# Optimization experiments

Measured on AMD Instinct MI355X. Metric: run time of the kernel, lower is better.

Reference implementation:

```python
import jax, jax.numpy as jnp
import numpy as np

N, E, D_IN, D_HID, D_OUT = 50000, 800000, 128, 128, 64

def setup_inputs() -> dict:
    key = jax.random.key(0)
    ks = jax.random.split(key, 20)
    inp = {
        'x': jax.random.normal(ks[0], (N, D_IN), dtype=jnp.float32),
        'edge_index': jax.random.randint(ks[1], (2, E), 0, N, dtype=jnp.int64),
        'edge_attr': jax.random.normal(ks[2], (E, 16), dtype=jnp.float32),
        'edge_weight': jax.random.uniform(ks[3], (E,), dtype=jnp.float32),
    }
    dims = [(D_IN, D_HID), (D_HID, D_HID), (D_HID, D_OUT)]
    for i, (di, do) in enumerate(dims):
        s = 1.0 / np.sqrt(di)
        inp[f'Wl{i}'] = jax.random.uniform(ks[4 + 5 * i], (di, do), minval=-s, maxval=s, dtype=jnp.float32)
        inp[f'bl{i}'] = jnp.zeros((do,), dtype=jnp.float32)
        inp[f'Wr{i}'] = jax.random.uniform(ks[5 + 5 * i], (di, do), minval=-s, maxval=s, dtype=jnp.float32)
        inp[f'Ws{i}'] = jax.random.uniform(ks[6 + 5 * i], (di, do), minval=-s, maxval=s, dtype=jnp.float32)
        inp[f'bs{i}'] = jnp.zeros((do,), dtype=jnp.float32)
    return inp


def _sage(x, src, dst, Wl, bl, Wr):
    # mean aggregation of source features at target nodes (PyG SAGEConv)
    msg = x[src]                                               # [E, d] gather
    ssum = jax.ops.segment_sum(msg, dst, num_segments=N)        # [N, d]
    cnt = jax.ops.segment_sum(jnp.ones((src.shape[0],), x.dtype), dst, num_segments=N)
    agg = ssum / jnp.maximum(cnt, 1.0)[:, None]
    return agg @ Wl + bl + x @ Wr                               # lin_l(agg) + lin_r(x)


def reference(x, edge_index, edge_attr, edge_weight,
              Wl0, bl0, Wr0, Ws0, bs0,
              Wl1, bl1, Wr1, Ws1, bs1,
              Wl2, bl2, Wr2, Ws2, bs2):
    src, dst = edge_index[0], edge_index[1]
    h = jax.nn.relu(_sage(x, src, dst, Wl0, bl0, Wr0) + x @ Ws0 + bs0)
    h = jax.nn.relu(_sage(h, src, dst, Wl1, bl1, Wr1) + h @ Ws1 + bs1)
    out = _sage(h, src, dst, Wl2, bl2, Wr2) + h @ Ws2 + bs2
    return out
```

## Files before the change

kernel.cpp:

```cpp
#include <hip/hip_runtime.h>
#include <hip/hip_bf16.h>


#define LB __launch_bounds__

typedef __attribute__((ext_vector_type(8))) short short8;
typedef __attribute__((ext_vector_type(4))) float f32x4;

__device__ __forceinline__ unsigned short bf16_rne(float f) {
  unsigned u = __builtin_bit_cast(unsigned, f);
  unsigned r = u + 0x7fffu + ((u >> 16) & 1u);
  return (unsigned short)(r >> 16);
}
__device__ __forceinline__ float bf16_to_f(unsigned short us) {
  return __builtin_bit_cast(float, (unsigned)us << 16);
}
__device__ __forceinline__ float bits_to_f(unsigned u) {
  return __builtin_bit_cast(float, u);
}

#define BCAP 8192
#define P1_CHUNK 4096

__global__ LB(256) void p1_bucket(const int* __restrict__ src, const int* __restrict__ dst,
                                  int* __restrict__ bcnt, int2* __restrict__ pairs, int E) {
  __shared__ int cnt[256];
  __shared__ int base[256];
  const int tid = threadIdx.x;
  cnt[tid] = 0;
  __syncthreads();
  const int e0 = blockIdx.x * P1_CHUNK;
  int myb[16], myr[16], mys[16], myd[16];
#pragma unroll
  for (int i = 0; i < 16; ++i) {
    int e = e0 + i * 256 + tid;
    myb[i] = -1;
    if (e < E) {
      int s = src[e], d = dst[e];
      int b = d >> 8;
      myb[i] = b;
      mys[i] = s;
      myd[i] = d;
      myr[i] = atomicAdd(&cnt[b], 1);
    }
  }
  __syncthreads();
  base[tid] = (cnt[tid] > 0) ? atomicAdd(&bcnt[tid], cnt[tid]) : 0;
  __syncthreads();
#pragma unroll
  for (int i = 0; i < 16; ++i) {
    int b = myb[i];
    if (b >= 0) {
      int p = base[b] + myr[i];
      if (p < BCAP) pairs[(size_t)b * BCAP + p] = make_int2(mys[i], myd[i]);
    }
  }
}

__global__ LB(256) void p234_kernel(const int2* __restrict__ pairs, const int* __restrict__ bcnt,
                                    int* __restrict__ gcounter, int* __restrict__ row_start,
                                    int* __restrict__ deg_arr, float* __restrict__ scale,
                                    int* __restrict__ srcs, int N) {
  __shared__ int h[256];
  __shared__ int sc[256];
  __shared__ int cur[256];
  __shared__ int shared_bb;
  const int tid = threadIdx.x;
  const int b = blockIdx.x;
  h[tid] = 0;
  __syncthreads();
  int m = bcnt[b];
  if (m > BCAP) m = BCAP;
  for (int i = tid; i < m; i += 256) {
    atomicAdd(&h[pairs[(size_t)b * BCAP + i].y & 255], 1);
  }
  __syncthreads();
  const int deg = h[tid];
  sc[tid] = deg;
  __syncthreads();
  for (int off = 1; off < 256; off <<= 1) {
    int add = (tid >= off) ? sc[tid - off] : 0;
    __syncthreads();
    sc[tid] += add;
    __syncthreads();
  }
  if (tid == 0) shared_bb = atomicAdd(gcounter, sc[255]);
  __syncthreads();
  const int abs_off = shared_bb + sc[tid] - deg;
  const int node = b * 256 + tid;
  if (node < N) {
    row_start[node] = abs_off;
    deg_arr[node] = deg;
    scale[node] = 1.0f / (float)(deg > 1 ? deg : 1);
  }
  cur[tid] = abs_off;
  __syncthreads();
  for (int i = tid; i < m; i += 256) {
    int2 pr = pairs[(size_t)b * BCAP + i];
    int p = atomicAdd(&cur[pr.y & 255], 1);
    srcs[p] = pr.x;
  }
}

__global__ LB(256) void wpack_all(const float* __restrict__ Wl0, const float* __restrict__ Wr0,
                                  const float* __restrict__ Ws0, const float* __restrict__ bl0,
                                  const float* __restrict__ bs0, const float* __restrict__ Wl1,
                                  const float* __restrict__ Wr1, const float* __restrict__ Ws1,
                                  const float* __restrict__ bl1, const float* __restrict__ bs1,
                                  const float* __restrict__ Wl2, const float* __restrict__ Wr2,
                                  const float* __restrict__ Ws2, const float* __restrict__ bl2,
                                  const float* __restrict__ bs2, ushort* __restrict__ Bh0,
                                  ushort* __restrict__ Bo0, float* __restrict__ bb0,
                                  ushort* __restrict__ Bh1, ushort* __restrict__ Bo1,
                                  float* __restrict__ bb1, ushort* __restrict__ Bh2,
                                  ushort* __restrict__ Bo2, float* __restrict__ bb2,
                                  int* __restrict__ bcnt, int* __restrict__ gcounter, int NB) {
  const int layer = blockIdx.y;
  if (layer == 0 && blockIdx.x == 0) {
    for (int i = threadIdx.x; i < NB; i += 256) bcnt[i] = 0;
    if (threadIdx.x == 0) *gcounter = 0;
  }
  const float *Wl, *Wr, *Ws, *bl, *bs;
  ushort *Bh, *Bo;
  float* bb;
  int M;
  if (layer == 0) {
    Wl = Wl0; Wr = Wr0; Ws = Ws0; bl = bl0; bs = bs0; Bh = Bh0; Bo = Bo0; bb = bb0; M = 256;
  } else if (layer == 1) {
    Wl = Wl1; Wr = Wr1; Ws = Ws1; bl = bl1; bs = bs1; Bh = Bh1; Bo = Bo1; bb = bb1; M = 256;
  } else {
    Wl = Wl2; Wr = Wr2; Ws = Ws2; bl = bl2; bs = bs2; Bh = Bh2; Bo = Bo2; bb = bb2; M = 128;
  }
  const int DO = M / 2;
  int idx = blockIdx.x * 256 + threadIdx.x;
  if (idx < 128 * M) {
    int k = idx / M, c = idx - k * M;
    float v = (c < DO) ? Wl[k * DO + c] : (Wr[k * DO + (c - DO)] + Ws[k * DO + (c - DO)]);
    unsigned short h = bf16_rne(v);
    unsigned short l = bf16_rne(v - bf16_to_f(h));
    int d = ((k >> 3) * M + c) * 8 + (k & 7);
    Bh[d] = h;
    Bo[d] = l;
  }
  if (idx < DO) bb[idx] = bl[idx] + bs[idx];
}

__device__ __forceinline__ void split8(const float* __restrict__ p, short8& h, short8& l) {
  float4 f0 = *(const float4*)p;
  float4 f1 = *(const float4*)(p + 4);
  float f[8] = {f0.x, f0.y, f0.z, f0.w, f1.x, f1.y, f1.z, f1.w};
#pragma unroll
  for (int j = 0; j < 8; ++j) {
    unsigned u = __builtin_bit_cast(unsigned, f[j]);
    h[j] = (short)(u >> 16);
    l[j] = (short)bf16_rne(f[j] - bits_to_f(u & 0xffff0000u));
  }
}

template <int M, bool AFP32>
__global__ LB(256, 4) void mfma_gemm_kernel(const float* __restrict__ Af,
                                            const ushort* __restrict__ Ahi,
                                            const ushort* __restrict__ Alo,
                                            const ushort* __restrict__ Bhi,
                                            const ushort* __restrict__ Blo,
                                            ushort* __restrict__ Yb, float* __restrict__ Z, int n) {
  constexpr int DO = M / 2;
  constexpr int NWC = (M >= 256) ? 4 : 2;
  constexpr int NWR = 4 / NWC;
  constexpr int BROWS = 32 * NWR;
  const int tid = threadIdx.x;
  const int w = tid >> 6, l = tid & 63;
  const int q = l >> 4, m16 = l & 15;
  const int rowBase = blockIdx.x * BROWS + (w / NWC) * 32;
  const int colBase = (w % NWC) * 64;

  f32x4 acc[2][4] = {};
  int rrow[2];
#pragma unroll
  for (int i = 0; i < 2; ++i) {
    int r = rowBase + i * 16 + m16;
    rrow[i] = r < n ? r : n - 1;
  }

#pragma unroll
  for (int s = 0; s < 4; ++s) {
    const int ka = s * 32 + q * 8;
    short8 ah[2], al[2], bh[4], bo[4];
#pragma unroll
    for (int i = 0; i < 2; ++i) {
      size_t off = (size_t)rrow[i] * 128 + ka;
      if (AFP32) {
        split8(Af + off, ah[i], al[i]);
      } else {
        ah[i] = *(const short8*)(Ahi + off);
        al[i] = *(const short8*)(Alo + off);
      }
    }
    const int kb = s * 4 + q;
#pragma unroll
    for (int j = 0; j < 4; ++j) {
      size_t off = ((size_t)kb * M + colBase + j * 16 + m16) * 8;
      bh[j] = *(const short8*)(Bhi + off);
      bo[j] = *(const short8*)(Blo + off);
    }
#pragma unroll
    for (int i = 0; i < 2; ++i)
#pragma unroll
      for (int j = 0; j < 4; ++j) {
        acc[i][j] = __builtin_amdgcn_mfma_f32_16x16x32_bf16(ah[i], bh[j], acc[i][j], 0, 0, 0);
        acc[i][j] = __builtin_amdgcn_mfma_f32_16x16x32_bf16(ah[i], bo[j], acc[i][j], 0, 0, 0);
        acc[i][j] = __builtin_amdgcn_mfma_f32_16x16x32_bf16(al[i], bh[j], acc[i][j], 0, 0, 0);
      }
  }

#pragma unroll
  for (int i = 0; i < 2; ++i) {
    int rb = rowBase + i * 16 + q * 4;
#pragma unroll
    for (int j = 0; j < 4; ++j) {
      int c = colBase + j * 16 + m16;
#pragma unroll
      for (int r = 0; r < 4; ++r) {
        int row = rb + r;
        if (row < n) {
          float v = acc[i][j][r];
          if (c < DO)
            Yb[(size_t)row * DO + c] = bf16_rne(v);
          else
            Z[(size_t)row * DO + (c - DO)] = v;
        }
      }
    }
  }
}

__global__ LB(256) void agg128_kernel(const ushort* __restrict__ Y, const float* __restrict__ Z,
                                      const int* __restrict__ row_start,
                                      const int* __restrict__ deg_arr, const int* __restrict__ srcs,
                                      const float* __restrict__ scale,
                                      const float* __restrict__ bsum, unsigned* __restrict__ Hhi,
                                      unsigned* __restrict__ Hlo, int n) {
  int node = blockIdx.x * 4 + (threadIdx.x >> 6);
  if (node >= n) return;
  const int lane = threadIdx.x & 63;
  const int li = lane & 31;
  const int half = lane >> 5;
  const int e0 = row_start[node];
  const int cnt = deg_arr[node];
  const int end = e0 + cnt;
  const int c1 = cnt < 64 ? cnt : 64;
  int idx = (lane < c1) ? srcs[e0 + lane] : 0;
  const uint2* Yu = (const uint2*)Y;
  float a0 = 0.f, a1 = 0.f, a2 = 0.f, a3 = 0.f;

  int j = 0;
  for (; j + 16 <= c1; j += 16) {
    int s[8];
#pragma unroll
    for (int t = 0; t < 8; ++t) s[t] = __shfl(idx, j + 2 * t + half);
    uint2 u[8];
#pragma unroll
    for (int t = 0; t < 8; ++t) u[t] = Yu[(size_t)s[t] * 32 + li];
#pragma unroll
    for (int t = 0; t < 8; ++t) {
      a0 += bits_to_f(u[t].x << 16);
      a1 += bits_to_f(u[t].x & 0xffff0000u);
      a2 += bits_to_f(u[t].y << 16);
      a3 += bits_to_f(u[t].y & 0xffff0000u);
    }
  }
  if (j + 8 <= c1) {
    int s[4];
#pragma unroll
    for (int t = 0; t < 4; ++t) s[t] = __shfl(idx, j + 2 * t + half);
    uint2 u[4];
#pragma unroll
    for (int t = 0; t < 4; ++t) u[t] = Yu[(size_t)s[t] * 32 + li];
#pragma unroll
    for (int t = 0; t < 4; ++t) {
      a0 += bits_to_f(u[t].x << 16);
      a1 += bits_to_f(u[t].x & 0xffff0000u);
      a2 += bits_to_f(u[t].y << 16);
      a3 += bits_to_f(u[t].y & 0xffff0000u);
    }
    j += 8;
  }
  for (; j + 2 <= c1; j += 2) {
    int s = __shfl(idx, j + half);
    uint2 u = Yu[(size_t)s * 32 + li];
    a0 += bits_to_f(u.x << 16);
    a1 += bits_to_f(u.x & 0xffff0000u);
    a2 += bits_to_f(u.y << 16);
    a3 += bits_to_f(u.y & 0xffff0000u);
  }
  if (j < c1) {
    int s = __shfl(idx, j);
    if (half == 0) {
      uint2 u = Yu[(size_t)s * 32 + li];
      a0 += bits_to_f(u.x << 16);
      a1 += bits_to_f(u.x & 0xffff0000u);
      a2 += bits_to_f(u.y << 16);
      a3 += bits_to_f(u.y & 0xffff0000u);
    }
  }
  if (cnt > 64) {
    int e = e0 + 64;
    for (; e + 2 <= end; e += 2) {
      int s = srcs[e + half];
      uint2 u = Yu[(size_t)s * 32 + li];
      a0 += bits_to_f(u.x << 16);
      a1 += bits_to_f(u.x & 0xffff0000u);
      a2 += bits_to_f(u.y << 16);
      a3 += bits_to_f(u.y & 0xffff0000u);
    }
    if (e < end && half == 0) {
      int s = srcs[e];
      uint2 u = Yu[(size_t)s * 32 + li];
      a0 += bits_to_f(u.x << 16);
      a1 += bits_to_f(u.x & 0xffff0000u);
      a2 += bits_to_f(u.y << 16);
      a3 += bits_to_f(u.y & 0xffff0000u);
    }
  }
  a0 += __shfl(a0, lane ^ 32);
  a1 += __shfl(a1, lane ^ 32);
  a2 += __shfl(a2, lane ^ 32);
  a3 += __shfl(a3, lane ^ 32);

  float sc = scale[node];
  float4 z = ((const float4*)Z)[(size_t)node * 32 + li];
  float4 b = ((const float4*)bsum)[li];
  float o0 = fmaxf(z.x + sc * a0 + b.x, 0.f);
  float o1 = fmaxf(z.y + sc * a1 + b.y, 0.f);
  float o2 = fmaxf(z.z + sc * a2 + b.z, 0.f);
  float o3 = fmaxf(z.w + sc * a3 + b.w, 0.f);
  unsigned short h0 = bf16_rne(o0), h1 = bf16_rne(o1), h2 = bf16_rne(o2), h3 = bf16_rne(o3);
  if (half == 0) {
    uint2 hp;
    hp.x = (unsigned)h0 | ((unsigned)h1 << 16);
    hp.y = (unsigned)h2 | ((unsigned)h3 << 16);
    ((uint2*)Hhi)[(size_t)node * 32 + li] = hp;
  } else {
    unsigned short l0 = bf16_rne(o0 - bf16_to_f(h0));
    unsigned short l1 = bf16_rne(o1 - bf16_to_f(h1));
    unsigned short l2 = bf16_rne(o2 - bf16_to_f(h2));
    unsigned short l3 = bf16_rne(o3 - bf16_to_f(h3));
    uint2 lp;
    lp.x = (unsigned)l0 | ((unsigned)l1 << 16);
    lp.y = (unsigned)l2 | ((unsigned)l3 << 16);
    ((uint2*)Hlo)[(size_t)node * 32 + li] = lp;
  }
}

__global__ LB(256) void agg64_kernel(const ushort* __restrict__ Y, const float* __restrict__ Z,
                                     const int* __restrict__ row_start,
                                     const int* __restrict__ deg_arr, const int* __restrict__ srcs,
                                     const float* __restrict__ scale, const float* __restrict__ bsum,
                                     float* __restrict__ out, int n) {
  int node = blockIdx.x * 4 + (threadIdx.x >> 6);
  if (node >= n) return;
  const int lane = threadIdx.x & 63;
  const int li = lane & 15;
  const int qt = lane >> 4;
  const int e0 = row_start[node];
  const int cnt = deg_arr[node];
  const int end = e0 + cnt;
  const int c1 = cnt < 64 ? cnt : 64;
  int idx = (lane < c1) ? srcs[e0 + lane] : 0;
  const uint2* Yu = (const uint2*)Y;
  float a0 = 0.f, a1 = 0.f, a2 = 0.f, a3 = 0.f;

  int j = 0;
  for (; j + 16 <= c1; j += 16) {
    int s0 = __shfl(idx, j + qt);
    int s1 = __shfl(idx, j + 4 + qt);
    int s2 = __shfl(idx, j + 8 + qt);
    int s3 = __shfl(idx, j + 12 + qt);
    uint2 u0 = Yu[(size_t)s0 * 16 + li];
    uint2 u1 = Yu[(size_t)s1 * 16 + li];
    uint2 u2 = Yu[(size_t)s2 * 16 + li];
    uint2 u3 = Yu[(size_t)s3 * 16 + li];
    a0 += bits_to_f(u0.x << 16) + bits_to_f(u1.x << 16) + bits_to_f(u2.x << 16) +
          bits_to_f(u3.x << 16);
    a1 += bits_to_f(u0.x & 0xffff0000u) + bits_to_f(u1.x & 0xffff0000u) +
          bits_to_f(u2.x & 0xffff0000u) + bits_to_f(u3.x & 0xffff0000u);
    a2 += bits_to_f(u0.y << 16) + bits_to_f(u1.y << 16) + bits_to_f(u2.y << 16) +
          bits_to_f(u3.y << 16);
    a3 += bits_to_f(u0.y & 0xffff0000u) + bits_to_f(u1.y & 0xffff0000u) +
          bits_to_f(u2.y & 0xffff0000u) + bits_to_f(u3.y & 0xffff0000u);
  }
  for (; j + 4 <= c1; j += 4) {
    int s = __shfl(idx, j + qt);
    uint2 u = Yu[(size_t)s * 16 + li];
    a0 += bits_to_f(u.x << 16);
    a1 += bits_to_f(u.x & 0xffff0000u);
    a2 += bits_to_f(u.y << 16);
    a3 += bits_to_f(u.y & 0xffff0000u);
  }
  {
    int rem = c1 - j;
    if (rem > 0) {
      int s = __shfl(idx, j + (qt < rem ? qt : 0));
      if (qt < rem) {
        uint2 u = Yu[(size_t)s * 16 + li];
        a0 += bits_to_f(u.x << 16);
        a1 += bits_to_f(u.x & 0xffff0000u);
        a2 += bits_to_f(u.y << 16);
        a3 += bits_to_f(u.y & 0xffff0000u);
      }
    }
  }
  if (cnt > 64) {
    int e = e0 + 64;
    for (; e + 4 <= end; e += 4) {
      int s = srcs[e + qt];
      uint2 u = Yu[(size_t)s * 16 + li];
      a0 += bits_to_f(u.x << 16);
      a1 += bits_to_f(u.x & 0xffff0000u);
      a2 += bits_to_f(u.y << 16);
      a3 += bits_to_f(u.y & 0xffff0000u);
    }
    int rem = end - e;
    if (qt < rem) {
      int s = srcs[e + qt];
      uint2 u = Yu[(size_t)s * 16 + li];
      a0 += bits_to_f(u.x << 16);
      a1 += bits_to_f(u.x & 0xffff0000u);
      a2 += bits_to_f(u.y << 16);
      a3 += bits_to_f(u.y & 0xffff0000u);
    }
  }
  a0 += __shfl(a0, lane ^ 16);
  a1 += __shfl(a1, lane ^ 16);
  a2 += __shfl(a2, lane ^ 16);
  a3 += __shfl(a3, lane ^ 16);
  a0 += __shfl(a0, lane ^ 32);
  a1 += __shfl(a1, lane ^ 32);
  a2 += __shfl(a2, lane ^ 32);
  a3 += __shfl(a3, lane ^ 32);

  if (qt == 0) {
    float sc = scale[node];
    float4 z = ((const float4*)Z)[(size_t)node * 16 + li];
    float4 b = ((const float4*)bsum)[li];
    float4 o;
    o.x = z.x + sc * a0 + b.x;
    o.y = z.y + sc * a1 + b.y;
    o.z = z.z + sc * a2 + b.z;
    o.w = z.w + sc * a3 + b.w;
    ((float4*)out)[(size_t)node * 16 + li] = o;
  }
}

extern "C" void kernel_launch(void* const* d_in, const int* in_sizes, int n_in,
                              void* d_out, int out_size, void* d_ws, size_t ws_size,
                              hipStream_t stream) {
  const float* x = (const float*)d_in[0];
  const int* ei = (const int*)d_in[1];
  const int N = in_sizes[0] / 128;
  const int E = in_sizes[3];
  const int* src = ei;
  const int* dst = ei + E;
  const float* Wl[3] = {(const float*)d_in[4], (const float*)d_in[9], (const float*)d_in[14]};
  const float* bl[3] = {(const float*)d_in[5], (const float*)d_in[10], (const float*)d_in[15]};
  const float* Wr[3] = {(const float*)d_in[6], (const float*)d_in[11], (const float*)d_in[16]};
  const float* Ws[3] = {(const float*)d_in[7], (const float*)d_in[12], (const float*)d_in[17]};
  const float* bs[3] = {(const float*)d_in[8], (const float*)d_in[13], (const float*)d_in[18]};

  const int NB = (N + 255) >> 8;

  size_t off = 0;
  auto carve = [&](size_t bytes) -> char* {
    char* p = (char*)d_ws + off;
    off += (bytes + 255) & ~(size_t)255;
    return p;
  };
  int* row_start = (int*)carve((size_t)N * 4);
  int* deg_arr = (int*)carve((size_t)N * 4);
  int* bcnt = (int*)carve((size_t)NB * 4);
  int* gcounter = (int*)carve(256);
  float* scale = (float*)carve((size_t)N * 4);
  int* srcs = (int*)carve((size_t)E * 4);
  int2* pairs = (int2*)carve((size_t)NB * BCAP * 8);
  ushort* Hhi = (ushort*)carve((size_t)N * 128 * 2);
  ushort* Hlo = (ushort*)carve((size_t)N * 128 * 2);
  ushort* Yb = (ushort*)carve((size_t)N * 128 * 2);
  float* Zf = (float*)carve((size_t)N * 128 * 4);
  ushort* Bh[3];
  ushort* Bo[3];
  float* bsum[3];
  for (int i = 0; i < 3; ++i) {
    Bh[i] = (ushort*)carve(128 * 256 * 2);
    Bo[i] = (ushort*)carve(128 * 256 * 2);
    bsum[i] = (float*)carve(128 * 4);
  }
  (void)ws_size;
  (void)n_in;
  (void)out_size;

  wpack_all<<<dim3(128, 3), 256, 0, stream>>>(Wl[0], Wr[0], Ws[0], bl[0], bs[0], Wl[1], Wr[1],
                                              Ws[1], bl[1], bs[1], Wl[2], Wr[2], Ws[2], bl[2],
                                              bs[2], Bh[0], Bo[0], bsum[0], Bh[1], Bo[1], bsum[1],
                                              Bh[2], Bo[2], bsum[2], bcnt, gcounter, NB);
  p1_bucket<<<(E + P1_CHUNK - 1) / P1_CHUNK, 256, 0, stream>>>(src, dst, bcnt, pairs, E);
  p234_kernel<<<NB, 256, 0, stream>>>(pairs, bcnt, gcounter, row_start, deg_arr, scale, srcs, N);

  int g32 = (N + 31) / 32;
  int g64 = (N + 63) / 64;
  int gAgg = (N + 3) / 4;

  mfma_gemm_kernel<256, true><<<g32, 256, 0, stream>>>(x, nullptr, nullptr, Bh[0], Bo[0], Yb, Zf, N);
  agg128_kernel<<<gAgg, 256, 0, stream>>>(Yb, Zf, row_start, deg_arr, srcs, scale, bsum[0],
                                          (unsigned*)Hhi, (unsigned*)Hlo, N);
  mfma_gemm_kernel<256, false><<<g32, 256, 0, stream>>>(nullptr, Hhi, Hlo, Bh[1], Bo[1], Yb, Zf, N);
  agg128_kernel<<<gAgg, 256, 0, stream>>>(Yb, Zf, row_start, deg_arr, srcs, scale, bsum[1],
                                          (unsigned*)Hhi, (unsigned*)Hlo, N);
  mfma_gemm_kernel<128, false><<<g64, 256, 0, stream>>>(nullptr, Hhi, Hlo, Bh[2], Bo[2], Yb, Zf, N);
  agg64_kernel<<<gAgg, 256, 0, stream>>>(Yb, Zf, row_start, deg_arr, srcs, scale, bsum[2],
                                         (float*)d_out, N);
}
```

Measured before the change: 329.5 us.

## Fuse preprocessing kernels and stage GEMM A tiles through LDS with async loads

Merges weight packing with edge bucketing, and CSR construction with the layer-0 GEMM, into combined launches that pick their role by block index. The counter zeroing moves to a hipMemsetAsync. GEMM A-operand rows are now staged into swizzled shared memory with global_load_lds async copies before the MFMA loop, and occupancy is lowered to 3 waves per SIMD to make room for that shared memory. The aim is to cut launch overhead and serialization between small kernels and to improve A-load coalescing, at the cost of extra LDS use and a barrier in each GEMM block.

```diff
diff --git a/kernel.cpp b/kernel.cpp
--- a/kernel.cpp
+++ b/kernel.cpp
@@ -19,17 +19,23 @@
   return __builtin_bit_cast(float, u);
 }
 
+__device__ __forceinline__ void async16(const void* g, void* l) {
+  __builtin_amdgcn_global_load_lds((const __attribute__((address_space(1))) unsigned*)g,
+                                   (__attribute__((address_space(3))) unsigned*)l, 16, 0, 0);
+}
+
 #define BCAP 8192
 #define P1_CHUNK 4096
 
-__global__ LB(256) void p1_bucket(const int* __restrict__ src, const int* __restrict__ dst,
-                                  int* __restrict__ bcnt, int2* __restrict__ pairs, int E) {
+__device__ __forceinline__ void p1_body(int bid, const int* __restrict__ src,
+                                        const int* __restrict__ dst, int* __restrict__ bcnt,
+                                        int2* __restrict__ pairs, int E) {
   __shared__ int cnt[256];
   __shared__ int base[256];
   const int tid = threadIdx.x;
   cnt[tid] = 0;
   __syncthreads();
-  const int e0 = blockIdx.x * P1_CHUNK;
+  const int e0 = bid * P1_CHUNK;
   int myb[16], myr[16], mys[16], myd[16];
 #pragma unroll
   for (int i = 0; i < 16; ++i) {
@@ -57,16 +63,15 @@
   }
 }
 
-__global__ LB(256) void p234_kernel(const int2* __restrict__ pairs, const int* __restrict__ bcnt,
-                                    int* __restrict__ gcounter, int* __restrict__ row_start,
-                                    int* __restrict__ deg_arr, float* __restrict__ scale,
-                                    int* __restrict__ srcs, int N) {
+__device__ __forceinline__ void p234_body(int b, const int2* __restrict__ pairs,
+                                          const int* __restrict__ bcnt, int* __restrict__ gcounter,
+                                          int* __restrict__ row_start, int* __restrict__ deg_arr,
+                                          float* __restrict__ scale, int* __restrict__ srcs, int N) {
   __shared__ int h[256];
   __shared__ int sc[256];
   __shared__ int cur[256];
   __shared__ int shared_bb;
   const int tid = threadIdx.x;
-  const int b = blockIdx.x;
   h[tid] = 0;
   __syncthreads();
   int m = bcnt[b];
@@ -102,24 +107,27 @@
   }
 }
 
-__global__ LB(256) void wpack_all(const float* __restrict__ Wl0, const float* __restrict__ Wr0,
-                                  const float* __restrict__ Ws0, const float* __restrict__ bl0,
-                                  const float* __restrict__ bs0, const float* __restrict__ Wl1,
-                                  const float* __restrict__ Wr1, const float* __restrict__ Ws1,
-                                  const float* __restrict__ bl1, const float* __restrict__ bs1,
-                                  const float* __restrict__ Wl2, const float* __restrict__ Wr2,
-                                  const float* __restrict__ Ws2, const float* __restrict__ bl2,
-                                  const float* __restrict__ bs2, ushort* __restrict__ Bh0,
-                                  ushort* __restrict__ Bo0, float* __restrict__ bb0,
-                                  ushort* __restrict__ Bh1, ushort* __restrict__ Bo1,
-                                  float* __restrict__ bb1, ushort* __restrict__ Bh2,
-                                  ushort* __restrict__ Bo2, float* __restrict__ bb2,
-                                  int* __restrict__ bcnt, int* __restrict__ gcounter, int NB) {
-  const int layer = blockIdx.y;
-  if (layer == 0 && blockIdx.x == 0) {
-    for (int i = threadIdx.x; i < NB; i += 256) bcnt[i] = 0;
-    if (threadIdx.x == 0) *gcounter = 0;
-  }
+__device__ __forceinline__ void wpack_body(int wb, const float* __restrict__ Wl0,
+                                           const float* __restrict__ Wr0,
+                                           const float* __restrict__ Ws0,
+                                           const float* __restrict__ bl0,
+                                           const float* __restrict__ bs0,
+                                           const float* __restrict__ Wl1,
+                                           const float* __restrict__ Wr1,
+                                           const float* __restrict__ Ws1,
+                                           const float* __restrict__ bl1,
+                                           const float* __restrict__ bs1,
+                                           const float* __restrict__ Wl2,
+                                           const float* __restrict__ Wr2,
+                                           const float* __restrict__ Ws2,
+                                           const float* __restrict__ bl2,
+                                           const float* __restrict__ bs2, ushort* __restrict__ Bh0,
+                                           ushort* __restrict__ Bo0, float* __restrict__ bb0,
+                                           ushort* __restrict__ Bh1, ushort* __restrict__ Bo1,
+                                           float* __restrict__ bb1, ushort* __restrict__ Bh2,
+                                           ushort* __restrict__ Bo2, float* __restrict__ bb2) {
+  const int layer = wb >> 7;
+  const int xb = wb & 127;
   const float *Wl, *Wr, *Ws, *bl, *bs;
   ushort *Bh, *Bo;
   float* bb;
@@ -132,7 +140,7 @@
     Wl = Wl2; Wr = Wr2; Ws = Ws2; bl = bl2; bs = bs2; Bh = Bh2; Bo = Bo2; bb = bb2; M = 128;
   }
   const int DO = M / 2;
-  int idx = blockIdx.x * 256 + threadIdx.x;
+  int idx = xb * 256 + (int)threadIdx.x;
   if (idx < 128 * M) {
     int k = idx / M, c = idx - k * M;
     float v = (c < DO) ? Wl[k * DO + c] : (Wr[k * DO + (c - DO)] + Ws[k * DO + (c - DO)]);
@@ -145,10 +153,8 @@
   if (idx < DO) bb[idx] = bl[idx] + bs[idx];
 }
 
-__device__ __forceinline__ void split8(const float* __restrict__ p, short8& h, short8& l) {
-  float4 f0 = *(const float4*)p;
-  float4 f1 = *(const float4*)(p + 4);
-  float f[8] = {f0.x, f0.y, f0.z, f0.w, f1.x, f1.y, f1.z, f1.w};
+__device__ __forceinline__ void split8v(f32x4 f0, f32x4 f1, short8& h, short8& l) {
+  float f[8] = {f0[0], f0[1], f0[2], f0[3], f1[0], f1[1], f1[2], f1[3]};
 #pragma unroll
   for (int j = 0; j < 8; ++j) {
     unsigned u = __builtin_bit_cast(unsigned, f[j]);
@@ -158,12 +164,12 @@
 }
 
 template <int M, bool AFP32>
-__global__ LB(256, 4) void mfma_gemm_kernel(const float* __restrict__ Af,
-                                            const ushort* __restrict__ Ahi,
-                                            const ushort* __restrict__ Alo,
-                                            const ushort* __restrict__ Bhi,
-                                            const ushort* __restrict__ Blo,
-                                            ushort* __restrict__ Yb, float* __restrict__ Z, int n) {
+__device__ __forceinline__ void gemm_body(int bx, const float* __restrict__ Af,
+                                          const ushort* __restrict__ Ahi,
+                                          const ushort* __restrict__ Alo,
+                                          const ushort* __restrict__ Bhi,
+                                          const ushort* __restrict__ Blo, ushort* __restrict__ Yb,
+                                          float* __restrict__ Z, int n, char* smem) {
   constexpr int DO = M / 2;
   constexpr int NWC = (M >= 256) ? 4 : 2;
   constexpr int NWR = 4 / NWC;
@@ -171,29 +177,55 @@
   const int tid = threadIdx.x;
   const int w = tid >> 6, l = tid & 63;
   const int q = l >> 4, m16 = l & 15;
-  const int rowBase = blockIdx.x * BROWS + (w / NWC) * 32;
+  const int blockRow0 = bx * BROWS;
+  const int rowBase = blockRow0 + (w / NWC) * 32;
   const int colBase = (w % NWC) * 64;
+  const int wbase = tid & ~63;
+
+  if (AFP32) {
+#pragma unroll
+    for (int r = 0; r < BROWS / 8; ++r) {
+      int ell = r * 256 + tid;
+      int row = ell >> 5, gl = ell & 31;
+      int grow = blockRow0 + row;
+      if (grow >= n) grow = n - 1;
+      int gs = gl ^ (row & 15);
+      async16(Af + (size_t)grow * 128 + gs * 4, smem + (size_t)(r * 256 + wbase) * 16);
+    }
+  } else {
+#pragma unroll
+    for (int r = 0; r < BROWS / 16; ++r) {
+      int ell = r * 256 + tid;
+      int row = ell >> 4, gl = ell & 15;
+      int grow = blockRow0 + row;
+      if (grow >= n) grow = n - 1;
+      int gs = gl ^ (row & 15);
+      async16(Ahi + (size_t)grow * 128 + gs * 8, smem + (size_t)(r * 256 + wbase) * 16);
+      async16(Alo + (size_t)grow * 128 + gs * 8,
+              smem + (size_t)BROWS * 256 + (size_t)(r * 256 + wbase) * 16);
+    }
+  }
+  __syncthreads();
 
   f32x4 acc[2][4] = {};
-  int rrow[2];
-#pragma unroll
-  for (int i = 0; i < 2; ++i) {
-    int r = rowBase + i * 16 + m16;
-    rrow[i] = r < n ? r : n - 1;
-  }
+  const int rl0 = (w / NWC) * 32 + m16;
 
 #pragma unroll
   for (int s = 0; s < 4; ++s) {
-    const int ka = s * 32 + q * 8;
     short8 ah[2], al[2], bh[4], bo[4];
 #pragma unroll
     for (int i = 0; i < 2; ++i) {
-      size_t off = (size_t)rrow[i] * 128 + ka;
+      int rl = rl0 + i * 16;
       if (AFP32) {
-        split8(Af + off, ah[i], al[i]);
+        int g0 = (2 * (s * 4 + q)) ^ m16;
+        int g1 = (2 * (s * 4 + q) + 1) ^ m16;
+        f32x4 fa = *(const f32x4*)(smem + (size_t)rl * 512 + g0 * 16);
+        f32x4 fb = *(const f32x4*)(smem + (size_t)rl * 512 + g1 * 16);
+        split8v(fa, fb, ah[i], al[i]);
       } else {
-        ah[i] = *(const short8*)(Ahi + off);
-        al[i] = *(const short8*)(Alo + off);
+        int g = (s * 4 + q) ^ m16;
+        ah[i] = *(const short8*)(smem + (size_t)rl * 256 + g * 16);
+        al[i] = *(const short8*)(smem + (size_t)BROWS * 256 + (size_t)rl * 256 + g * 16);
       }
     }
     const int kb = s * 4 + q;
@@ -231,6 +263,52 @@
         }
       }
     }
+  }
+}
+
+template <int M, bool AFP32>
+__global__ LB(256, 3) void mfma_gemm_kernel(const float* __restrict__ Af,
+                                            const ushort* __restrict__ Ahi,
+                                            const ushort* __restrict__ Alo,
+                                            const ushort* __restrict__ Bhi,
+                                            const ushort* __restrict__ Blo,
+                                            ushort* __restrict__ Yb, float* __restrict__ Z, int n) {
+  constexpr int LDSB = AFP32 ? (32 * 512) : ((M >= 256 ? 32 : 64) * 512);
+  __shared__ __align__(16) char smem[LDSB];
+  gemm_body<M, AFP32>(blockIdx.x, Af, Ahi, Alo, Bhi, Blo, Yb, Z, n, smem);
+}
+
+__global__ LB(256) void fused_wpack_p1(const int* __restrict__ src, const int* __restrict__ dst,
+                                       int* __restrict__ bcnt, int2* __restrict__ pairs, int E,
+                                       int NP1, const float* Wl0, const float* Wr0, const float* Ws0,
+                                       const float* bl0, const float* bs0, const float* Wl1,
+                                       const float* Wr1, const float* Ws1, const float* bl1,
+                                       const float* bs1, const float* Wl2, const float* Wr2,
+                                       const float* Ws2, const float* bl2, const float* bs2,
+                                       ushort* Bh0, ushort* Bo0, float* bb0, ushort* Bh1,
+                                       ushort* Bo1, float* bb1, ushort* Bh2, ushort* Bo2,
+                                       float* bb2) {
+  if ((int)blockIdx.x < NP1) {
+    p1_body(blockIdx.x, src, dst, bcnt, pairs, E);
+  } else {
+    wpack_body(blockIdx.x - NP1, Wl0, Wr0, Ws0, bl0, bs0, Wl1, Wr1, Ws1, bl1, bs1, Wl2, Wr2, Ws2,
+               bl2, bs2, Bh0, Bo0, bb0, Bh1, Bo1, bb1, Bh2, Bo2, bb2);
+  }
+}
+
+__global__ LB(256, 3) void fused_p234_gemm0(const int2* __restrict__ pairs,
+                                            const int* __restrict__ bcnt, int* __restrict__ gcounter,
+                                            int* __restrict__ row_start, int* __restrict__ deg_arr,
+                                            float* __restrict__ scale, int* __restrict__ srcs, int N,
+                                            const float* __restrict__ x,
+                                            const ushort* __restrict__ Bh0,
+                                            const ushort* __restrict__ Bo0, ushort* __restrict__ Yb,
+                                            float* __restrict__ Zf, int NB) {
+  __shared__ __align__(16) char smem[32 * 512];
+  if ((int)blockIdx.x < NB) {
+    p234_body(blockIdx.x, pairs, bcnt, gcounter, row_start, deg_arr, scale, srcs, N);
+  } else {
+    gemm_body<256, true>(blockIdx.x - NB, x, nullptr, nullptr, Bh0, Bo0, Yb, Zf, N, smem);
   }
 }
 
@@ -468,6 +546,7 @@
   const float* bs[3] = {(const float*)d_in[8], (const float*)d_in[13], (const float*)d_in[18]};
 
   const int NB = (N + 255) >> 8;
+  const int NP1 = (E + P1_CHUNK - 1) / P1_CHUNK;
 
   size_t off = 0;
   auto carve = [&](size_t bytes) -> char* {
@@ -498,18 +577,20 @@
   (void)n_in;
   (void)out_size;
 
-  wpack_all<<<dim3(128, 3), 256, 0, stream>>>(Wl[0], Wr[0], Ws[0], bl[0], bs[0], Wl[1], Wr[1],
-                                              Ws[1], bl[1], bs[1], Wl[2], Wr[2], Ws[2], bl[2],
-                                              bs[2], Bh[0], Bo[0], bsum[0], Bh[1], Bo[1], bsum[1],
-                                              Bh[2], Bo[2], bsum[2], bcnt, gcounter, NB);
-  p1_bucket<<<(E + P1_CHUNK - 1) / P1_CHUNK, 256, 0, stream>>>(src, dst, bcnt, pairs, E);
-  p234_kernel<<<NB, 256, 0, stream>>>(pairs, bcnt, gcounter, row_start, deg_arr, scale, srcs, N);
+  size_t bcnt_pad = ((size_t)NB * 4 + 255) & ~(size_t)255;
+  hipMemsetAsync(bcnt, 0, bcnt_pad + 4, stream);
+
+  fused_wpack_p1<<<NP1 + 384, 256, 0, stream>>>(
+      src, dst, bcnt, pairs, E, NP1, Wl[0], Wr[0], Ws[0], bl[0], bs[0], Wl[1], Wr[1], Ws[1], bl[1],
+      bs[1], Wl[2], Wr[2], Ws[2], bl[2], bs[2], Bh[0], Bo[0], bsum[0], Bh[1], Bo[1], bsum[1], Bh[2],
+      Bo[2], bsum[2]);
 
   int g32 = (N + 31) / 32;
   int g64 = (N + 63) / 64;
   int gAgg = (N + 3) / 4;
 
-  mfma_gemm_kernel<256, true><<<g32, 256, 0, stream>>>(x, nullptr, nullptr, Bh[0], Bo[0], Yb, Zf, N);
+  fused_p234_gemm0<<<NB + g32, 256, 0, stream>>>(pairs, bcnt, gcounter, row_start, deg_arr, scale,
+                                                 srcs, N, x, Bh[0], Bo[0], Yb, Zf, NB);
   agg128_kernel<<<gAgg, 256, 0, stream>>>(Yb, Zf, row_start, deg_arr, srcs, scale, bsum[0],
                                           (unsigned*)Hhi, (unsigned*)Hlo, N);
   mfma_gemm_kernel<256, false><<<g32, 256, 0, stream>>>(nullptr, Hhi, Hlo, Bh[1], Bo[1], Yb, Zf, N);
```

Result: faster. 301.9 us (-8.4%).
